# Performance work log

Hardware: AMD Instinct MI355X
Metric: run time of the kernel (lower is better)

The kernel has to match this reference:

```python
import jax, jax.numpy as jnp
import numpy as np

H, N, B, L = 512, 32, 8, 4096
DT_MIN, DT_MAX = 1e-3, 1e-1

def setup_inputs() -> dict:
    key = jax.random.key(0)
    k_u, k_dt, k_C, k_D = jax.random.split(key, 4)
    u = jax.random.normal(k_u, (B, H, L), dtype=jnp.float32)
    # log_dt ~ Uniform(log dt_min, log dt_max)
    log_dt = np.log(DT_MIN) + jax.random.uniform(k_dt, (H,), dtype=jnp.float32) * (np.log(DT_MAX) - np.log(DT_MIN))
    # A_re = -0.5 -> log(-A_re) = log(0.5)
    log_neg_A_re = jnp.full((H, N), np.log(0.5), dtype=jnp.float32)
    n = jnp.arange(N, dtype=jnp.float32)
    a_im = (2.0 * N / np.pi) * (2.0 * N / (2.0 * n + 1.0) - 1.0)
    A_im = jnp.broadcast_to(a_im, (H, N)).astype(jnp.float32)
    # B = 1 + 0j, stored as real/imag pair
    B_ri = jnp.stack([jnp.ones((H, N), jnp.float32), jnp.zeros((H, N), jnp.float32)], axis=-1)
    # C ~ complex standard normal, bidirectional -> leading dim 2
    C_ri = jax.random.normal(k_C, (2, H, N, 2), dtype=jnp.float32)
    D = jax.random.normal(k_D, (H,), dtype=jnp.float32)
    return {"u": u, "log_dt": log_dt, "log_neg_A_re": log_neg_A_re,
            "A_im": A_im, "B_ri": B_ri, "C_ri": C_ri, "D": D}

def reference(u, log_dt, log_neg_A_re, A_im, B_ri, C_ri, D):
    Lx = u.shape[-1]
    dt = jnp.exp(log_dt)                                   # [H]
    A = -jnp.exp(log_neg_A_re) + 1j * A_im                 # [H, N] complex
    Bc = B_ri[..., 0] + 1j * B_ri[..., 1]                  # [H, N]
    Cc = C_ri[..., 0] + 1j * C_ri[..., 1]                  # [2, H, N]
    C = Cc * Bc                                            # [2, H, N]
    dtA = dt[:, None] * A                                  # [H, N]
    C = C * (jnp.exp(dtA) - 1.0) / A                       # ZOH-like discretization
    # log-Vandermonde reduction: K[c,h,l] = 2*Re(sum_n C[c,h,n] * exp(dtA[h,n]*l))
    l = jnp.arange(Lx, dtype=jnp.float32)
    V = jnp.exp(dtA[:, :, None] * l)                       # [H, N, L] complex
    K = 2.0 * jnp.real(jnp.einsum('chn,hnl->chl', C, V))   # [2, H, L]
    # bidirectional: causal kernel + anticausal (flipped) kernel, length 2L
    k0, k1 = K[0], K[1]
    z = jnp.zeros_like(k0)
    Kfull = jnp.concatenate([k0, z], axis=-1) + jnp.concatenate([z, k1[..., ::-1]], axis=-1)  # [H, 2L]
    # FFT long convolution
    k_f = jnp.fft.rfft(Kfull, n=2 * Lx)                    # [H, L+1]
    u_f = jnp.fft.rfft(u, n=2 * Lx)                        # [B, H, L+1]
    y = jnp.fft.irfft(u_f * k_f, n=2 * Lx)[..., :Lx]       # [B, H, L]
    return y + u * D[:, None]
```

## Files before the change

### kernel.cpp

```cpp
#include <hip/hip_runtime.h>
#include <math.h>

#define Hn 512
#define Nn 32
#define Bn 8
#define Ln 4096
#define NF 4096
#define NT 256
#define ROWF 4097
#define TWOPI 6.28318530717958647692f

__device__ __forceinline__ float2 cmulf(float2 a, float2 b) {
    return make_float2(a.x * b.x - a.y * b.y, a.x * b.y + a.y * b.x);
}
__device__ __forceinline__ float2 caddf(float2 a, float2 b) { return make_float2(a.x + b.x, a.y + b.y); }
__device__ __forceinline__ float2 csubf(float2 a, float2 b) { return make_float2(a.x - b.x, a.y - b.y); }

__device__ __forceinline__ int SW(int a) { return a ^ ((a >> 5) & 31); }
__device__ __forceinline__ int pos4(int k) { return ((k & 15) << 8) | (((k >> 4) & 15) << 4) | ((k >> 8) & 15); }

__device__ __forceinline__ float2 ldz(const float* ZR, const float* ZI, int a) {
    int s = SW(a);
    return make_float2(ZR[s], ZI[s]);
}
__device__ __forceinline__ void stz(float* ZR, float* ZI, int a, float2 v) {
    int s = SW(a);
    ZR[s] = v.x;
    ZI[s] = v.y;
}

template <int SGN>
__device__ __forceinline__ void dft4(float2& a0, float2& a1, float2& a2, float2& a3) {
    float2 t0 = caddf(a0, a2), t1 = csubf(a0, a2);
    float2 t2 = caddf(a1, a3), t3 = csubf(a1, a3);
    float2 it3 = (SGN < 0) ? make_float2(t3.y, -t3.x) : make_float2(-t3.y, t3.x);
    a0 = caddf(t0, t2);
    a2 = csubf(t0, t2);
    a1 = caddf(t1, it3);
    a3 = csubf(t1, it3);
}

template <int SGN, bool ZTOP>
__device__ __forceinline__ void dft16(float2* x) {
    const float C1 = 0.92387953251128675613f, S1 = 0.38268343236508977173f, R2 = 0.70710678118654752440f;
    const float sg = (SGN < 0) ? -1.f : 1.f;
    if (ZTOP) {
#pragma unroll
        for (int q = 0; q < 4; ++q) {
            float2 xa = x[q], xb = x[q + 4];
            float2 it3 = (SGN < 0) ? make_float2(xb.y, -xb.x) : make_float2(-xb.y, xb.x);
            x[q] = caddf(xa, xb);
            x[q + 8] = csubf(xa, xb);
            x[q + 4] = caddf(xa, it3);
            x[q + 12] = csubf(xa, it3);
        }
    } else {
#pragma unroll
        for (int q = 0; q < 4; ++q) dft4<SGN>(x[q], x[q + 4], x[q + 8], x[q + 12]);
    }
    const float2 w1 = make_float2(C1, sg * S1);
    const float2 w2 = make_float2(R2, sg * R2);
    const float2 w3 = make_float2(S1, sg * C1);
    const float2 w6 = make_float2(-R2, sg * R2);
    const float2 w9 = make_float2(-C1, -sg * S1);
    x[5] = cmulf(x[5], w1);
    x[9] = cmulf(x[9], w2);
    x[13] = cmulf(x[13], w3);
    x[6] = cmulf(x[6], w2);
    x[10] = make_float2(-sg * x[10].y, sg * x[10].x);
    x[14] = cmulf(x[14], w6);
    x[7] = cmulf(x[7], w3);
    x[11] = cmulf(x[11], w6);
    x[15] = cmulf(x[15], w9);
#pragma unroll
    for (int a = 0; a < 4; ++a) dft4<SGN>(x[4 * a + 0], x[4 * a + 1], x[4 * a + 2], x[4 * a + 3]);
}

template <int SGN, bool TW>
__device__ void stage_lds(float* ZR, float* ZI, int base, int stride, float tau) {
    float2 x[16];
#pragma unroll
    for (int p = 0; p < 16; ++p) x[p] = ldz(ZR, ZI, base + stride * p);
    if (SGN < 0) {
        dft16<SGN, false>(x);
        if (TW) {
            float s, c;
            __sincosf(TWOPI * tau, &s, &c);
            float2 w1 = make_float2(c, -s);
            float2 w = w1;
            stz(ZR, ZI, base, x[0]);
#pragma unroll
            for (int r = 1; r < 16; ++r) {
                int sl = ((r & 3) << 2) | (r >> 2);
                stz(ZR, ZI, base + stride * r, cmulf(x[sl], w));
                w = cmulf(w, w1);
            }
        } else {
#pragma unroll
            for (int r = 0; r < 16; ++r) {
                int sl = ((r & 3) << 2) | (r >> 2);
                stz(ZR, ZI, base + stride * r, x[sl]);
            }
        }
    } else {
        if (TW) {
            float s, c;
            __sincosf(TWOPI * tau, &s, &c);
            float2 w1 = make_float2(c, s);
            float2 w = w1;
#pragma unroll
            for (int r = 1; r < 16; ++r) {
                x[r] = cmulf(x[r], w);
                w = cmulf(w, w1);
            }
        }
        dft16<SGN, false>(x);
#pragma unroll
        for (int n = 0; n < 16; ++n) {
            int sl = ((n & 3) << 2) | (n >> 2);
            stz(ZR, ZI, base + stride * n, x[sl]);
        }
    }
}

__device__ __forceinline__ void scatterA(float* ZR, float* ZI, int j, float2* x) {
    float s, c;
    __sincosf(TWOPI * (float)j * (1.f / 4096.f), &s, &c);
    float2 w1 = make_float2(c, -s);
    float2 w = w1;
    stz(ZR, ZI, j, x[0]);
#pragma unroll
    for (int r = 1; r < 16; ++r) {
        int sl = ((r & 3) << 2) | (r >> 2);
        stz(ZR, ZI, j + 256 * r, cmulf(x[sl], w));
        w = cmulf(w, w1);
    }
}

__device__ __forceinline__ void pointwise_pair(float* ZR, float* ZI, int k, float2 KA, float2 KB) {
    int pk = pos4(k), pm = pos4((NF - k) & (NF - 1));
    float2 Xk = ldz(ZR, ZI, pk), Xm = ldz(ZR, ZI, pm);
    float2 E = make_float2(0.5f * (Xk.x + Xm.x), 0.5f * (Xk.y - Xm.y));
    float2 O = make_float2(0.5f * (Xk.y + Xm.y), -0.5f * (Xk.x - Xm.x));
    float s, c;
    __sincosf(-TWOPI * (float)k * (1.f / 8192.f), &s, &c);
    float2 P = cmulf(make_float2(c, s), O);
    float2 Vk = caddf(E, P);
    float2 Vm = make_float2(E.x - P.x, -(E.y - P.y));
    float2 Yk = cmulf(Vk, KA);
    float2 Ym = cmulf(Vm, KB);
    float2 Ze = make_float2(0.5f * (Yk.x + Ym.x), 0.5f * (Yk.y - Ym.y));
    float2 T = make_float2(0.5f * (Yk.x - Ym.x), 0.5f * (Yk.y + Ym.y));
    float2 Zo = make_float2(c * T.x + s * T.y, c * T.y - s * T.x);
    stz(ZR, ZI, pk, make_float2(Ze.x - Zo.y, Ze.y + Zo.x));
    stz(ZR, ZI, pm, make_float2(Ze.x + Zo.y, -Ze.y + Zo.x));
}

__global__ __launch_bounds__(NT, 2) void k_fftk(const float* __restrict__ log_dt,
                                                const float* __restrict__ lnA,
                                                const float* __restrict__ A_im,
                                                const float* __restrict__ B_ri,
                                                const float* __restrict__ C_ri,
                                                const float* __restrict__ D,
                                                float2* __restrict__ KF) {
    __shared__ float ZR[NF];
    __shared__ float ZI[NF];
    __shared__ float CST[Nn][14];
    int h = blockIdx.x, j = threadIdx.x;
    if (j < Nn) {
        int n = j, idx = h * Nn + n;
        float dt = __expf(log_dt[h]);
        float are = -__expf(lnA[idx]);
        float aim = A_im[idx];
        float dre = dt * are;
        double taud = fmod((double)dt * (double)aim * 0.15915494309189533577, 1.0);
        if (taud < 0.0) taud += 1.0;
        float tau_hi = truncf((float)taud * 4096.f) * (1.f / 4096.f);
        float tau_lo = (float)(taud - (double)tau_hi);
        float s0, c0;
        __sincosf(TWOPI * (float)taud, &s0, &c0);
        float er = __expf(dre);
        float2 w = make_float2(er * c0, er * s0);
        float inv2 = 1.f / (are * are + aim * aim);
        float2 num = make_float2(w.x - 1.f, w.y);
        float2 disc = make_float2((num.x * are + num.y * aim) * inv2,
                                  (num.y * are - num.x * aim) * inv2);
        float2 Bc = make_float2(B_ri[2 * idx], B_ri[2 * idx + 1]);
        float2 CB = cmulf(Bc, disc);
        int i1 = Hn * Nn + idx;
        float2 cA = cmulf(make_float2(C_ri[2 * idx], C_ri[2 * idx + 1]), CB);
        cA.x *= 2.f; cA.y *= 2.f;
        float2 cC = cmulf(make_float2(C_ri[2 * i1], C_ri[2 * i1 + 1]), CB);
        cC.x *= 2.f; cC.y *= 2.f;
        float2 cB2 = cmulf(cA, w);
        float einv = __expf(-2.f * dre);
        float2 winv = make_float2(w.x * einv, -w.y * einv);
        float2 cD = cmulf(cC, winv);
        double t512 = fmod(512.0 * taud, 1.0);
        float e512 = __expf(512.f * dre);
        float sR, cR;
        __sincosf(TWOPI * (float)t512, &sR, &cR);
        CST[n][0] = cA.x;  CST[n][1] = cA.y;
        CST[n][2] = cB2.x; CST[n][3] = cB2.y;
        CST[n][4] = cC.x;  CST[n][5] = cC.y;
        CST[n][6] = cD.x;  CST[n][7] = cD.y;
        CST[n][8] = e512 * cR; CST[n][9] = e512 * sR;
        CST[n][10] = dre; CST[n][11] = tau_hi; CST[n][12] = tau_lo;
    }
    __syncthreads();
    {
        float2 acc[8];
#pragma unroll
        for (int p = 0; p < 8; ++p) acc[p] = make_float2(0.f, 0.f);
        float l_lo = (float)(2 * j);
        for (int n = 0; n < Nn; ++n) {
            float2 cA = make_float2(CST[n][0], CST[n][1]);
            float2 cB2 = make_float2(CST[n][2], CST[n][3]);
            float2 R = make_float2(CST[n][8], CST[n][9]);
            float dre = CST[n][10], thi = CST[n][11], tlo = CST[n][12];
            float ph = l_lo * thi;
            ph -= floorf(ph);
            ph += l_lo * tlo;
            ph -= floorf(ph);
            float s, c;
            __sincosf(TWOPI * ph, &s, &c);
            float m0 = __expf(dre * l_lo);
            float2 q = make_float2(m0 * c, m0 * s);
#pragma unroll
            for (int p = 0; p < 8; ++p) {
                acc[p].x += cA.x * q.x - cA.y * q.y;
                acc[p].y += cB2.x * q.x - cB2.y * q.y;
                q = cmulf(q, R);
            }
        }
#pragma unroll
        for (int p = 0; p < 8; ++p) stz(ZR, ZI, j + 256 * p, acc[p]);
    }
    float2 x[16];
    {
        float2 acc[8];
#pragma unroll
        for (int p = 0; p < 8; ++p) acc[p] = make_float2(0.f, 0.f);
        float l_hi = (float)(511 - 2 * j);
        for (int n = 0; n < Nn; ++n) {
            float2 cC = make_float2(CST[n][4], CST[n][5]);
            float2 cD = make_float2(CST[n][6], CST[n][7]);
            float2 R = make_float2(CST[n][8], CST[n][9]);
            float dre = CST[n][10], thi = CST[n][11], tlo = CST[n][12];
            float ph2 = l_hi * thi;
            ph2 -= floorf(ph2);
            ph2 += l_hi * tlo;
            ph2 -= floorf(ph2);
            float s2, c2;
            __sincosf(TWOPI * ph2, &s2, &c2);
            float m1 = __expf(dre * l_hi);
            float2 r = make_float2(m1 * c2, m1 * s2);
#pragma unroll
            for (int p = 7; p >= 0; --p) {
                acc[p].x += cC.x * r.x - cC.y * r.y;
                acc[p].y += cD.x * r.x - cD.y * r.y;
                r = cmulf(r, R);
            }
        }
#pragma unroll
        for (int p = 0; p < 8; ++p) x[8 + p] = acc[p];
    }
#pragma unroll
    for (int p = 0; p < 8; ++p) x[p] = ldz(ZR, ZI, j + 256 * p);
    dft16<-1, false>(x);
    scatterA(ZR, ZI, j, x);
    __syncthreads();
    stage_lds<-1, true>(ZR, ZI, ((j >> 4) << 8) | (j & 15), 16, (float)(j & 15) * (1.f / 256.f));
    __syncthreads();
    stage_lds<-1, false>(ZR, ZI, j << 4, 1, 0.f);
    __syncthreads();
    float Dh = D[h];
    const float inv = 1.f / 4096.f;
    float2* row = KF + (size_t)h * ROWF;
#pragma unroll
    for (int jj = 0; jj < 8; ++jj) {
        int k = ((j & 7) << 8) | (jj << 5) | (j >> 3);
        int pk = pos4(k), pm = pos4((NF - k) & (NF - 1));
        float2 Xk = ldz(ZR, ZI, pk), Xm = ldz(ZR, ZI, pm);
        float2 E = make_float2(0.5f * (Xk.x + Xm.x), 0.5f * (Xk.y - Xm.y));
        float2 O = make_float2(0.5f * (Xk.y + Xm.y), -0.5f * (Xk.x - Xm.x));
        float s, c;
        __sincosf(-TWOPI * (float)k * (1.f / 8192.f), &s, &c);
        float2 P = cmulf(make_float2(c, s), O);
        row[jj * 256 + j] = make_float2((E.x + P.x + Dh) * inv, (E.y + P.y) * inv);
        row[2048 + jj * 256 + j] = make_float2((E.x - P.x + Dh) * inv, -(E.y - P.y) * inv);
    }
    if (j == NT - 1) {
        float2 Xk = ldz(ZR, ZI, pos4(2048));
        row[4096] = make_float2((Xk.x + Dh) * inv, -Xk.y * inv);
    }
}

__global__ __launch_bounds__(NT, 4) void k_conv(const float* __restrict__ u,
                                                const float2* __restrict__ KF,
                                                float* __restrict__ y) {
    __shared__ float ZR[NF];
    __shared__ float ZI[NF];
    int wg = blockIdx.x;
    int h = wg & 511, b = wg >> 9;
    int j = threadIdx.x;
    const float2* u2 = (const float2*)(u + ((size_t)b * Hn + h) * Ln);
    float2 x[16];
#pragma unroll
    for (int p = 0; p < 8; ++p) x[p] = u2[j + 256 * p];
    dft16<-1, true>(x);
    scatterA(ZR, ZI, j, x);
    __syncthreads();
    stage_lds<-1, true>(ZR, ZI, ((j >> 4) << 8) | (j & 15), 16, (float)(j & 15) * (1.f / 256.f));
    __syncthreads();
    stage_lds<-1, false>(ZR, ZI, j << 4, 1, 0.f);
    __syncthreads();
    const float2* row = KF + (size_t)h * ROWF;
#pragma unroll
    for (int jj = 0; jj < 8; ++jj) {
        int k = ((j & 7) << 8) | (jj << 5) | (j >> 3);
        pointwise_pair(ZR, ZI, k, row[jj * 256 + j], row[2048 + jj * 256 + j]);
    }
    if (j == NT - 1) pointwise_pair(ZR, ZI, 2048, row[4096], row[4096]);
    __syncthreads();
    stage_lds<1, false>(ZR, ZI, j << 4, 1, 0.f);
    __syncthreads();
    stage_lds<1, true>(ZR, ZI, ((j >> 4) << 8) | (j & 15), 16, (float)(j & 15) * (1.f / 256.f));
    __syncthreads();
    float2 xx[16];
#pragma unroll
    for (int p = 0; p < 16; ++p) xx[p] = ldz(ZR, ZI, j + 256 * p);
    {
        float s, c;
        __sincosf(TWOPI * (float)j * (1.f / 4096.f), &s, &c);
        float2 w1 = make_float2(c, s);
        float2 w = w1;
#pragma unroll
        for (int r = 1; r < 16; ++r) {
            xx[r] = cmulf(xx[r], w);
            w = cmulf(w, w1);
        }
    }
    dft16<1, false>(xx);
    float2* y2 = (float2*)(y + ((size_t)b * Hn + h) * Ln);
#pragma unroll
    for (int n = 0; n < 8; ++n) {
        int sl = ((n & 3) << 2) | (n >> 2);
        y2[j + 256 * n] = xx[sl];
    }
}

extern "C" void kernel_launch(void* const* d_in, const int* in_sizes, int n_in,
                              void* d_out, int out_size, void* d_ws, size_t ws_size,
                              hipStream_t stream) {
    const float* u = (const float*)d_in[0];
    const float* log_dt = (const float*)d_in[1];
    const float* lnA = (const float*)d_in[2];
    const float* A_im = (const float*)d_in[3];
    const float* B_ri = (const float*)d_in[4];
    const float* C_ri = (const float*)d_in[5];
    const float* D = (const float*)d_in[6];
    float* y = (float*)d_out;
    float2* KF = (float2*)d_ws;

    k_fftk<<<Hn, NT, 0, stream>>>(log_dt, lnA, A_im, B_ri, C_ri, D, KF);
    k_conv<<<Bn * Hn, NT, 0, stream>>>(u, KF, y);
}
```

Baseline: 188.8 us.

## Split kernel generation from FFT into separate launches with doubled grid

The fused kernel-generation and FFT kernel is split in two. A new k_gen kernel runs 2*H workgroups, one half for the causal and one for the anticausal Vandermonde sums, under higher launch bounds so more blocks fit per CU. A separate k_fft kernel reads those values back from the workspace and performs the FFT. This exposes more parallelism in the sincos/exp-heavy generation phase, at the cost of an extra launch and a global-memory round trip, and each H row's constants are now set up twice.

```diff
diff --git a/kernel.cpp b/kernel.cpp
--- a/kernel.cpp
+++ b/kernel.cpp
@@ -156,17 +156,12 @@
     stz(ZR, ZI, pm, make_float2(Ze.x + Zo.y, -Ze.y + Zo.x));
 }
 
-__global__ __launch_bounds__(NT, 2) void k_fftk(const float* __restrict__ log_dt,
-                                                const float* __restrict__ lnA,
-                                                const float* __restrict__ A_im,
-                                                const float* __restrict__ B_ri,
-                                                const float* __restrict__ C_ri,
-                                                const float* __restrict__ D,
-                                                float2* __restrict__ KF) {
-    __shared__ float ZR[NF];
-    __shared__ float ZI[NF];
-    __shared__ float CST[Nn][14];
-    int h = blockIdx.x, j = threadIdx.x;
+__device__ __forceinline__ void setup_cst(float CST[Nn][14], int h, int j,
+                                          const float* __restrict__ log_dt,
+                                          const float* __restrict__ lnA,
+                                          const float* __restrict__ A_im,
+                                          const float* __restrict__ B_ri,
+                                          const float* __restrict__ C_ri) {
     if (j < Nn) {
         int n = j, idx = h * Nn + n;
         float dt = __expf(log_dt[h]);
@@ -207,11 +202,27 @@
         CST[n][8] = e512 * cR; CST[n][9] = e512 * sR;
         CST[n][10] = dre; CST[n][11] = tau_hi; CST[n][12] = tau_lo;
     }
-    __syncthreads();
-    {
-        float2 acc[8];
-#pragma unroll
-        for (int p = 0; p < 8; ++p) acc[p] = make_float2(0.f, 0.f);
+}
+
+__global__ __launch_bounds__(NT, 4) void k_gen(const float* __restrict__ log_dt,
+                                               const float* __restrict__ lnA,
+                                               const float* __restrict__ A_im,
+                                               const float* __restrict__ B_ri,
+                                               const float* __restrict__ C_ri,
+                                               float2* __restrict__ KT) {
+    __shared__ float CST[Nn][14];
+    int wg = blockIdx.x;
+    int h = wg & 511, q = wg >> 9;
+    int j = threadIdx.x;
+    setup_cst(CST, h, j, log_dt, lnA, A_im, B_ri, C_ri);
+    __syncthreads();
+
+    float2 acc[8];
+#pragma unroll
+    for (int p = 0; p < 8; ++p) acc[p] = make_float2(0.f, 0.f);
+    float2* row = KT + (size_t)h * ROWF;
+
+    if (q == 0) {
         float l_lo = (float)(2 * j);
         for (int n = 0; n < Nn; ++n) {
             float2 cA = make_float2(CST[n][0], CST[n][1]);
@@ -225,22 +236,17 @@
             float s, c;
             __sincosf(TWOPI * ph, &s, &c);
             float m0 = __expf(dre * l_lo);
-            float2 q = make_float2(m0 * c, m0 * s);
+            float2 qv = make_float2(m0 * c, m0 * s);
 #pragma unroll
             for (int p = 0; p < 8; ++p) {
-                acc[p].x += cA.x * q.x - cA.y * q.y;
-                acc[p].y += cB2.x * q.x - cB2.y * q.y;
-                q = cmulf(q, R);
-            }
-        }
-#pragma unroll
-        for (int p = 0; p < 8; ++p) stz(ZR, ZI, j + 256 * p, acc[p]);
-    }
-    float2 x[16];
-    {
-        float2 acc[8];
-#pragma unroll
-        for (int p = 0; p < 8; ++p) acc[p] = make_float2(0.f, 0.f);
+                acc[p].x += cA.x * qv.x - cA.y * qv.y;
+                acc[p].y += cB2.x * qv.x - cB2.y * qv.y;
+                qv = cmulf(qv, R);
+            }
+        }
+#pragma unroll
+        for (int p = 0; p < 8; ++p) row[j + 256 * p] = acc[p];
+    } else {
         float l_hi = (float)(511 - 2 * j);
         for (int n = 0; n < Nn; ++n) {
             float2 cC = make_float2(CST[n][4], CST[n][5]);
@@ -263,10 +269,19 @@
             }
         }
 #pragma unroll
-        for (int p = 0; p < 8; ++p) x[8 + p] = acc[p];
-    }
-#pragma unroll
-    for (int p = 0; p < 8; ++p) x[p] = ldz(ZR, ZI, j + 256 * p);
+        for (int p = 0; p < 8; ++p) row[j + 256 * (8 + p)] = acc[p];
+    }
+}
+
+__global__ __launch_bounds__(NT, 2) void k_fft(const float* __restrict__ D,
+                                               float2* __restrict__ KF) {
+    __shared__ float ZR[NF];
+    __shared__ float ZI[NF];
+    int h = blockIdx.x, j = threadIdx.x;
+    float2* row = KF + (size_t)h * ROWF;
+    float2 x[16];
+#pragma unroll
+    for (int p = 0; p < 16; ++p) x[p] = row[j + 256 * p];
     dft16<-1, false>(x);
     scatterA(ZR, ZI, j, x);
     __syncthreads();
@@ -276,7 +291,6 @@
     __syncthreads();
     float Dh = D[h];
     const float inv = 1.f / 4096.f;
-    float2* row = KF + (size_t)h * ROWF;
 #pragma unroll
     for (int jj = 0; jj < 8; ++jj) {
         int k = ((j & 7) << 8) | (jj << 5) | (j >> 3);
@@ -363,6 +377,7 @@
     float* y = (float*)d_out;
     float2* KF = (float2*)d_ws;
 
-    k_fftk<<<Hn, NT, 0, stream>>>(log_dt, lnA, A_im, B_ri, C_ri, D, KF);
+    k_gen<<<2 * Hn, NT, 0, stream>>>(log_dt, lnA, A_im, B_ri, C_ri, KF);
+    k_fft<<<Hn, NT, 0, stream>>>(D, KF);
     k_conv<<<Bn * Hn, NT, 0, stream>>>(u, KF, y);
 }
```

New measurement: 192.3 us. About the same (+1.8%).

## Vectorize complex math with packed float2 FMAs and recurrence twiddles

Applied to the files above, without the earlier changes.

Replaces the float2 struct helpers with a 2-wide ext_vector complex type so complex multiplies and adds can map to packed FMA instructions. In the pointwise and kernel-post stages, per-element sincos twiddles are replaced by one sincos plus repeated multiplication by a fixed step. The 0.5 factors are folded into the kernel normalization (1/16384), and the Vandermonde accumulation is restructured as two vector FMAs per term. k_conv's launch bound goes from 4 to 5 blocks per SM. The twiddle recurrence can accumulate rounding error, and the tighter register limit from the new launch bound may cause spills.

```diff
diff --git a/kernel.cpp b/kernel.cpp
--- a/kernel.cpp
+++ b/kernel.cpp
@@ -10,64 +10,70 @@
 #define ROWF 4097
 #define TWOPI 6.28318530717958647692f
 
-__device__ __forceinline__ float2 cmulf(float2 a, float2 b) {
-    return make_float2(a.x * b.x - a.y * b.y, a.x * b.y + a.y * b.x);
-}
-__device__ __forceinline__ float2 caddf(float2 a, float2 b) { return make_float2(a.x + b.x, a.y + b.y); }
-__device__ __forceinline__ float2 csubf(float2 a, float2 b) { return make_float2(a.x - b.x, a.y - b.y); }
+typedef float cplx __attribute__((ext_vector_type(2)));
+
+__device__ __forceinline__ cplx cmulf(cplx a, cplx b) {
+    cplx bsw = __builtin_shufflevector(b, b, 1, 0);
+    cplx asw = __builtin_shufflevector(-a, a, 1, 3);
+    return __builtin_elementwise_fma(asw, bsw, a.x * b);
+}
+__device__ __forceinline__ cplx cconj(cplx a) { return (cplx){a.x, -a.y}; }
+__device__ __forceinline__ cplx cswap(cplx a) { return __builtin_shufflevector(a, a, 1, 0); }
+__device__ __forceinline__ cplx mulI(cplx a) { return __builtin_shufflevector(-a, a, 1, 2); }
+__device__ __forceinline__ cplx mulNegI(cplx a) { return __builtin_shufflevector(a, -a, 1, 2); }
 
 __device__ __forceinline__ int SW(int a) { return a ^ ((a >> 5) & 31); }
 __device__ __forceinline__ int pos4(int k) { return ((k & 15) << 8) | (((k >> 4) & 15) << 4) | ((k >> 8) & 15); }
 
-__device__ __forceinline__ float2 ldz(const float* ZR, const float* ZI, int a) {
+__device__ __forceinline__ cplx ldz(const float* ZR, const float* ZI, int a) {
     int s = SW(a);
-    return make_float2(ZR[s], ZI[s]);
-}
-__device__ __forceinline__ void stz(float* ZR, float* ZI, int a, float2 v) {
+    return (cplx){ZR[s], ZI[s]};
+}
+__device__ __forceinline__ void stz(float* ZR, float* ZI, int a, cplx v) {
     int s = SW(a);
     ZR[s] = v.x;
     ZI[s] = v.y;
 }
 
 template <int SGN>
-__device__ __forceinline__ void dft4(float2& a0, float2& a1, float2& a2, float2& a3) {
-    float2 t0 = caddf(a0, a2), t1 = csubf(a0, a2);
-    float2 t2 = caddf(a1, a3), t3 = csubf(a1, a3);
-    float2 it3 = (SGN < 0) ? make_float2(t3.y, -t3.x) : make_float2(-t3.y, t3.x);
-    a0 = caddf(t0, t2);
-    a2 = csubf(t0, t2);
-    a1 = caddf(t1, it3);
-    a3 = csubf(t1, it3);
+__device__ __forceinline__ void dft4(cplx& a0, cplx& a1, cplx& a2, cplx& a3) {
+    cplx t0 = a0 + a2, t1 = a0 - a2;
+    cplx t2 = a1 + a3, t3 = a1 - a3;
+    cplx it3 = (SGN < 0) ? mulNegI(t3) : mulI(t3);
+    a0 = t0 + t2;
+    a2 = t0 - t2;
+    a1 = t1 + it3;
+    a3 = t1 - it3;
 }
 
 template <int SGN, bool ZTOP>
-__device__ __forceinline__ void dft16(float2* x) {
+__device__ __forceinline__ void dft16(cplx* x) {
     const float C1 = 0.92387953251128675613f, S1 = 0.38268343236508977173f, R2 = 0.70710678118654752440f;
     const float sg = (SGN < 0) ? -1.f : 1.f;
     if (ZTOP) {
 #pragma unroll
         for (int q = 0; q < 4; ++q) {
-            float2 xa = x[q], xb = x[q + 4];
-            float2 it3 = (SGN < 0) ? make_float2(xb.y, -xb.x) : make_float2(-xb.y, xb.x);
-            x[q] = caddf(xa, xb);
-            x[q + 8] = csubf(xa, xb);
-            x[q + 4] = caddf(xa, it3);
-            x[q + 12] = csubf(xa, it3);
+            cplx xa = x[q], xb = x[q + 4];
+            cplx it3 = (SGN < 0) ? mulNegI(xb) : mulI(xb);
+            x[q] = xa + xb;
+            x[q + 8] = xa - xb;
+            x[q + 4] = xa + it3;
+            x[q + 12] = xa - it3;
         }
     } else {
 #pragma unroll
         for (int q = 0; q < 4; ++q) dft4<SGN>(x[q], x[q + 4], x[q + 8], x[q + 12]);
     }
-    const float2 w1 = make_float2(C1, sg * S1);
-    const float2 w2 = make_float2(R2, sg * R2);
-    const float2 w3 = make_float2(S1, sg * C1);
-    const float2 w6 = make_float2(-R2, sg * R2);
-    const float2 w9 = make_float2(-C1, -sg * S1);
+    const cplx w1 = {C1, sg * S1};
+    const cplx w2 = {R2, sg * R2};
+    const cplx w3 = {S1, sg * C1};
+    const cplx w6 = {-R2, sg * R2};
+    const cplx w9 = {-C1, -sg * S1};
     x[5] = cmulf(x[5], w1);
     x[9] = cmulf(x[9], w2);
     x[13] = cmulf(x[13], w3);
     x[6] = cmulf(x[6], w2);
-    x[10] = make_float2(-sg * x[10].y, sg * x[10].x);
+    x[10] = (SGN < 0) ? mulNegI(x[10]) : mulI(x[10]);
     x[14] = cmulf(x[14], w6);
     x[7] = cmulf(x[7], w3);
     x[11] = cmulf(x[11], w6);
@@ -78,7 +84,7 @@
 
 template <int SGN, bool TW>
 __device__ void stage_lds(float* ZR, float* ZI, int base, int stride, float tau) {
-    float2 x[16];
+    cplx x[16];
 #pragma unroll
     for (int p = 0; p < 16; ++p) x[p] = ldz(ZR, ZI, base + stride * p);
     if (SGN < 0) {
@@ -86,8 +92,8 @@
         if (TW) {
             float s, c;
             __sincosf(TWOPI * tau, &s, &c);
-            float2 w1 = make_float2(c, -s);
-            float2 w = w1;
+            cplx w1 = {c, -s};
+            cplx w = w1;
             stz(ZR, ZI, base, x[0]);
 #pragma unroll
             for (int r = 1; r < 16; ++r) {
@@ -106,8 +112,8 @@
         if (TW) {
             float s, c;
             __sincosf(TWOPI * tau, &s, &c);
-            float2 w1 = make_float2(c, s);
-            float2 w = w1;
+            cplx w1 = {c, s};
+            cplx w = w1;
 #pragma unroll
             for (int r = 1; r < 16; ++r) {
                 x[r] = cmulf(x[r], w);
@@ -123,11 +129,11 @@
     }
 }
 
-__device__ __forceinline__ void scatterA(float* ZR, float* ZI, int j, float2* x) {
+__device__ __forceinline__ void scatterA(float* ZR, float* ZI, int j, cplx* x) {
     float s, c;
     __sincosf(TWOPI * (float)j * (1.f / 4096.f), &s, &c);
-    float2 w1 = make_float2(c, -s);
-    float2 w = w1;
+    cplx w1 = {c, -s};
+    cplx w = w1;
     stz(ZR, ZI, j, x[0]);
 #pragma unroll
     for (int r = 1; r < 16; ++r) {
@@ -137,24 +143,26 @@
     }
 }
 
-__device__ __forceinline__ void pointwise_pair(float* ZR, float* ZI, int k, float2 KA, float2 KB) {
-    int pk = pos4(k), pm = pos4((NF - k) & (NF - 1));
-    float2 Xk = ldz(ZR, ZI, pk), Xm = ldz(ZR, ZI, pm);
-    float2 E = make_float2(0.5f * (Xk.x + Xm.x), 0.5f * (Xk.y - Xm.y));
-    float2 O = make_float2(0.5f * (Xk.y + Xm.y), -0.5f * (Xk.x - Xm.x));
-    float s, c;
-    __sincosf(-TWOPI * (float)k * (1.f / 8192.f), &s, &c);
-    float2 P = cmulf(make_float2(c, s), O);
-    float2 Vk = caddf(E, P);
-    float2 Vm = make_float2(E.x - P.x, -(E.y - P.y));
-    float2 Yk = cmulf(Vk, KA);
-    float2 Ym = cmulf(Vm, KB);
-    float2 Ze = make_float2(0.5f * (Yk.x + Ym.x), 0.5f * (Yk.y - Ym.y));
-    float2 T = make_float2(0.5f * (Yk.x - Ym.x), 0.5f * (Yk.y + Ym.y));
-    float2 Zo = make_float2(c * T.x + s * T.y, c * T.y - s * T.x);
-    stz(ZR, ZI, pk, make_float2(Ze.x - Zo.y, Ze.y + Zo.x));
-    stz(ZR, ZI, pm, make_float2(Ze.x + Zo.y, -Ze.y + Zo.x));
-}
+__device__ __forceinline__ void pointwise_pair(float* ZR, float* ZI, int pk, int pm,
+                                               cplx w, cplx KA, cplx KB) {
+    cplx Xk = ldz(ZR, ZI, pk), Xm = ldz(ZR, ZI, pm);
+    cplx Xmc = cconj(Xm);
+    cplx E = Xk + Xmc;
+    cplx O = mulNegI(Xk - Xmc);
+    cplx P = cmulf(w, O);
+    cplx Vk = E + P;
+    cplx Vm = cconj(E - P);
+    cplx Yk = cmulf(Vk, KA);
+    cplx Ym = cmulf(Vm, KB);
+    cplx Ymc = cconj(Ym);
+    cplx Ze = Yk + Ymc;
+    cplx T = Yk - Ymc;
+    cplx Zo = cmulf(cconj(w), T);
+    stz(ZR, ZI, pk, Ze + mulI(Zo));
+    stz(ZR, ZI, pm, cconj(Ze) + cswap(Zo));
+}
+
+#define WSTEP ((cplx){0.99969881869620422f, -0.024541228522912288f})
 
 __global__ __launch_bounds__(NT, 2) void k_fftk(const float* __restrict__ log_dt,
                                                 const float* __restrict__ lnA,
@@ -162,7 +170,7 @@
                                                 const float* __restrict__ B_ri,
                                                 const float* __restrict__ C_ri,
                                                 const float* __restrict__ D,
-                                                float2* __restrict__ KF) {
+                                                cplx* __restrict__ KF) {
     __shared__ float ZR[NF];
     __shared__ float ZI[NF];
     __shared__ float CST[Nn][14];
@@ -180,43 +188,43 @@
         float s0, c0;
         __sincosf(TWOPI * (float)taud, &s0, &c0);
         float er = __expf(dre);
-        float2 w = make_float2(er * c0, er * s0);
+        cplx w = {er * c0, er * s0};
         float inv2 = 1.f / (are * are + aim * aim);
-        float2 num = make_float2(w.x - 1.f, w.y);
-        float2 disc = make_float2((num.x * are + num.y * aim) * inv2,
-                                  (num.y * are - num.x * aim) * inv2);
-        float2 Bc = make_float2(B_ri[2 * idx], B_ri[2 * idx + 1]);
-        float2 CB = cmulf(Bc, disc);
+        cplx num = {w.x - 1.f, w.y};
+        cplx disc = {(num.x * are + num.y * aim) * inv2,
+                     (num.y * are - num.x * aim) * inv2};
+        cplx Bc = {B_ri[2 * idx], B_ri[2 * idx + 1]};
+        cplx CB = cmulf(Bc, disc);
         int i1 = Hn * Nn + idx;
-        float2 cA = cmulf(make_float2(C_ri[2 * idx], C_ri[2 * idx + 1]), CB);
-        cA.x *= 2.f; cA.y *= 2.f;
-        float2 cC = cmulf(make_float2(C_ri[2 * i1], C_ri[2 * i1 + 1]), CB);
-        cC.x *= 2.f; cC.y *= 2.f;
-        float2 cB2 = cmulf(cA, w);
+        cplx cA = cmulf((cplx){C_ri[2 * idx], C_ri[2 * idx + 1]}, CB);
+        cA = 2.f * cA;
+        cplx cC = cmulf((cplx){C_ri[2 * i1], C_ri[2 * i1 + 1]}, CB);
+        cC = 2.f * cC;
+        cplx cB2 = cmulf(cA, w);
         float einv = __expf(-2.f * dre);
-        float2 winv = make_float2(w.x * einv, -w.y * einv);
-        float2 cD = cmulf(cC, winv);
+        cplx winv = {w.x * einv, -w.y * einv};
+        cplx cD = cmulf(cC, winv);
         double t512 = fmod(512.0 * taud, 1.0);
         float e512 = __expf(512.f * dre);
         float sR, cR;
         __sincosf(TWOPI * (float)t512, &sR, &cR);
-        CST[n][0] = cA.x;  CST[n][1] = cA.y;
-        CST[n][2] = cB2.x; CST[n][3] = cB2.y;
-        CST[n][4] = cC.x;  CST[n][5] = cC.y;
-        CST[n][6] = cD.x;  CST[n][7] = cD.y;
+        CST[n][0] = cA.x;   CST[n][1] = cB2.x;
+        CST[n][2] = -cA.y;  CST[n][3] = -cB2.y;
+        CST[n][4] = cC.x;   CST[n][5] = cD.x;
+        CST[n][6] = -cC.y;  CST[n][7] = -cD.y;
         CST[n][8] = e512 * cR; CST[n][9] = e512 * sR;
         CST[n][10] = dre; CST[n][11] = tau_hi; CST[n][12] = tau_lo;
     }
     __syncthreads();
     {
-        float2 acc[8];
-#pragma unroll
-        for (int p = 0; p < 8; ++p) acc[p] = make_float2(0.f, 0.f);
+        cplx acc[8];
+#pragma unroll
+        for (int p = 0; p < 8; ++p) acc[p] = (cplx){0.f, 0.f};
         float l_lo = (float)(2 * j);
         for (int n = 0; n < Nn; ++n) {
-            float2 cA = make_float2(CST[n][0], CST[n][1]);
-            float2 cB2 = make_float2(CST[n][2], CST[n][3]);
-            float2 R = make_float2(CST[n][8], CST[n][9]);
+            cplx P1 = {CST[n][0], CST[n][1]};
+            cplx P2 = {CST[n][2], CST[n][3]};
+            cplx R = {CST[n][8], CST[n][9]};
             float dre = CST[n][10], thi = CST[n][11], tlo = CST[n][12];
             float ph = l_lo * thi;
             ph -= floorf(ph);
@@ -225,27 +233,27 @@
             float s, c;
             __sincosf(TWOPI * ph, &s, &c);
             float m0 = __expf(dre * l_lo);
-            float2 q = make_float2(m0 * c, m0 * s);
+            cplx qv = {m0 * c, m0 * s};
 #pragma unroll
             for (int p = 0; p < 8; ++p) {
-                acc[p].x += cA.x * q.x - cA.y * q.y;
-                acc[p].y += cB2.x * q.x - cB2.y * q.y;
-                q = cmulf(q, R);
+                acc[p] = __builtin_elementwise_fma(qv.xx, P1,
+                         __builtin_elementwise_fma(qv.yy, P2, acc[p]));
+                qv = cmulf(qv, R);
             }
         }
 #pragma unroll
         for (int p = 0; p < 8; ++p) stz(ZR, ZI, j + 256 * p, acc[p]);
     }
-    float2 x[16];
-    {
-        float2 acc[8];
-#pragma unroll
-        for (int p = 0; p < 8; ++p) acc[p] = make_float2(0.f, 0.f);
+    cplx x[16];
+    {
+        cplx acc[8];
+#pragma unroll
+        for (int p = 0; p < 8; ++p) acc[p] = (cplx){0.f, 0.f};
         float l_hi = (float)(511 - 2 * j);
         for (int n = 0; n < Nn; ++n) {
-            float2 cC = make_float2(CST[n][4], CST[n][5]);
-            float2 cD = make_float2(CST[n][6], CST[n][7]);
-            float2 R = make_float2(CST[n][8], CST[n][9]);
+            cplx P3 = {CST[n][4], CST[n][5]};
+            cplx P4 = {CST[n][6], CST[n][7]};
+            cplx R = {CST[n][8], CST[n][9]};
             float dre = CST[n][10], thi = CST[n][11], tlo = CST[n][12];
             float ph2 = l_hi * thi;
             ph2 -= floorf(ph2);
@@ -254,11 +262,11 @@
             float s2, c2;
             __sincosf(TWOPI * ph2, &s2, &c2);
             float m1 = __expf(dre * l_hi);
-            float2 r = make_float2(m1 * c2, m1 * s2);
+            cplx r = {m1 * c2, m1 * s2};
 #pragma unroll
             for (int p = 7; p >= 0; --p) {
-                acc[p].x += cC.x * r.x - cC.y * r.y;
-                acc[p].y += cD.x * r.x - cD.y * r.y;
+                acc[p] = __builtin_elementwise_fma(r.xx, P3,
+                         __builtin_elementwise_fma(r.yy, P4, acc[p]));
                 r = cmulf(r, R);
             }
         }
@@ -275,37 +283,45 @@
     stage_lds<-1, false>(ZR, ZI, j << 4, 1, 0.f);
     __syncthreads();
     float Dh = D[h];
-    const float inv = 1.f / 4096.f;
-    float2* row = KF + (size_t)h * ROWF;
-#pragma unroll
-    for (int jj = 0; jj < 8; ++jj) {
-        int k = ((j & 7) << 8) | (jj << 5) | (j >> 3);
-        int pk = pos4(k), pm = pos4((NF - k) & (NF - 1));
-        float2 Xk = ldz(ZR, ZI, pk), Xm = ldz(ZR, ZI, pm);
-        float2 E = make_float2(0.5f * (Xk.x + Xm.x), 0.5f * (Xk.y - Xm.y));
-        float2 O = make_float2(0.5f * (Xk.y + Xm.y), -0.5f * (Xk.x - Xm.x));
+    const float inv = 1.f / 16384.f;
+    const cplx dterm = {Dh * inv, 0.f};
+    const cplx half_inv = {0.5f * inv, 0.5f * inv};
+    cplx* row = KF + (size_t)h * ROWF;
+    {
+        int k0 = ((j & 7) << 8) | (j >> 3);
         float s, c;
-        __sincosf(-TWOPI * (float)k * (1.f / 8192.f), &s, &c);
-        float2 P = cmulf(make_float2(c, s), O);
-        row[jj * 256 + j] = make_float2((E.x + P.x + Dh) * inv, (E.y + P.y) * inv);
-        row[2048 + jj * 256 + j] = make_float2((E.x - P.x + Dh) * inv, -(E.y - P.y) * inv);
+        __sincosf(-TWOPI * (float)k0 * (1.f / 8192.f), &s, &c);
+        cplx w = {c, s};
+#pragma unroll
+        for (int jj = 0; jj < 8; ++jj) {
+            int k = k0 | (jj << 5);
+            int pk = pos4(k), pm = pos4((NF - k) & (NF - 1));
+            cplx Xk = ldz(ZR, ZI, pk), Xm = ldz(ZR, ZI, pm);
+            cplx Xmc = cconj(Xm);
+            cplx E = Xk + Xmc;
+            cplx O = mulNegI(Xk - Xmc);
+            cplx P = cmulf(w, O);
+            row[jj * 256 + j] = __builtin_elementwise_fma(E + P, half_inv, dterm);
+            row[2048 + jj * 256 + j] = cconj((E - P) * half_inv) + dterm;
+            w = cmulf(w, WSTEP);
+        }
     }
     if (j == NT - 1) {
-        float2 Xk = ldz(ZR, ZI, pos4(2048));
-        row[4096] = make_float2((Xk.x + Dh) * inv, -Xk.y * inv);
-    }
-}
-
-__global__ __launch_bounds__(NT, 4) void k_conv(const float* __restrict__ u,
-                                                const float2* __restrict__ KF,
+        cplx Xk = ldz(ZR, ZI, pos4(2048));
+        row[4096] = (cplx){(Xk.x + Dh) * inv, -Xk.y * inv};
+    }
+}
+
+__global__ __launch_bounds__(NT, 5) void k_conv(const float* __restrict__ u,
+                                                const cplx* __restrict__ KF,
                                                 float* __restrict__ y) {
     __shared__ float ZR[NF];
     __shared__ float ZI[NF];
     int wg = blockIdx.x;
     int h = wg & 511, b = wg >> 9;
     int j = threadIdx.x;
-    const float2* u2 = (const float2*)(u + ((size_t)b * Hn + h) * Ln);
-    float2 x[16];
+    const cplx* u2 = (const cplx*)(u + ((size_t)b * Hn + h) * Ln);
+    cplx x[16];
 #pragma unroll
     for (int p = 0; p < 8; ++p) x[p] = u2[j + 256 * p];
     dft16<-1, true>(x);
@@ -315,26 +331,37 @@
     __syncthreads();
     stage_lds<-1, false>(ZR, ZI, j << 4, 1, 0.f);
     __syncthreads();
-    const float2* row = KF + (size_t)h * ROWF;
-#pragma unroll
-    for (int jj = 0; jj < 8; ++jj) {
-        int k = ((j & 7) << 8) | (jj << 5) | (j >> 3);
-        pointwise_pair(ZR, ZI, k, row[jj * 256 + j], row[2048 + jj * 256 + j]);
-    }
-    if (j == NT - 1) pointwise_pair(ZR, ZI, 2048, row[4096], row[4096]);
+    const cplx* row = KF + (size_t)h * ROWF;
+    {
+        int k0 = ((j & 7) << 8) | (j >> 3);
+        float s, c;
+        __sincosf(-TWOPI * (float)k0 * (1.f / 8192.f), &s, &c);
+        cplx w = {c, s};
+#pragma unroll
+        for (int jj = 0; jj < 8; ++jj) {
+            int k = k0 | (jj << 5);
+            int pk = pos4(k), pm = pos4((NF - k) & (NF - 1));
+            pointwise_pair(ZR, ZI, pk, pm, w, row[jj * 256 + j], row[2048 + jj * 256 + j]);
+            w = cmulf(w, WSTEP);
+        }
+    }
+    if (j == NT - 1) {
+        int p2 = pos4(2048);
+        pointwise_pair(ZR, ZI, p2, p2, (cplx){0.f, -1.f}, row[4096], row[4096]);
+    }
     __syncthreads();
     stage_lds<1, false>(ZR, ZI, j << 4, 1, 0.f);
     __syncthreads();
     stage_lds<1, true>(ZR, ZI, ((j >> 4) << 8) | (j & 15), 16, (float)(j & 15) * (1.f / 256.f));
     __syncthreads();
-    float2 xx[16];
+    cplx xx[16];
 #pragma unroll
     for (int p = 0; p < 16; ++p) xx[p] = ldz(ZR, ZI, j + 256 * p);
     {
         float s, c;
         __sincosf(TWOPI * (float)j * (1.f / 4096.f), &s, &c);
-        float2 w1 = make_float2(c, s);
-        float2 w = w1;
+        cplx w1 = {c, s};
+        cplx w = w1;
 #pragma unroll
         for (int r = 1; r < 16; ++r) {
             xx[r] = cmulf(xx[r], w);
@@ -342,7 +369,7 @@
         }
     }
     dft16<1, false>(xx);
-    float2* y2 = (float2*)(y + ((size_t)b * Hn + h) * Ln);
+    cplx* y2 = (cplx*)(y + ((size_t)b * Hn + h) * Ln);
 #pragma unroll
     for (int n = 0; n < 8; ++n) {
         int sl = ((n & 3) << 2) | (n >> 2);
@@ -361,7 +388,7 @@
     const float* C_ri = (const float*)d_in[5];
     const float* D = (const float*)d_in[6];
     float* y = (float*)d_out;
-    float2* KF = (float2*)d_ws;
+    cplx* KF = (cplx*)d_ws;
 
     k_fftk<<<Hn, NT, 0, stream>>>(log_dt, lnA, A_im, B_ri, C_ri, D, KF);
     k_conv<<<Bn * Hn, NT, 0, stream>>>(u, KF, y);
```

New measurement: 215.7 us. 1.14x slower.
